# Optimization experiments

Measured on AMD Instinct MI355X. Metric: run time of the kernel, lower is better.

## Reference

```python
import jax, jax.numpy as jnp
import numpy as np

# ---- dims ----
B, NP_, NL = 32, 350, 30          # graphs, protein atoms, ligand atoms per graph
NG = NP_ + NL
N = B * NG                        # 12160 nodes
E = B * NP_ * NL                  # 336000 edges (dense bipartite per graph)
HID, HEADS, G = 128, 16, 20
DH = HID // HEADS
KV = 2 * HID + G                  # 276
R_MIN, R_MAX = 0.0, 10.0


def _mlp_params(key, din, dout, hid=HID):
    k1, k2 = jax.random.split(key)
    return (jax.random.normal(k1, (din, hid), jnp.float32) / np.sqrt(din),
            jnp.zeros((hid,), jnp.float32),
            jnp.ones((hid,), jnp.float32),
            jnp.zeros((hid,), jnp.float32),
            jax.random.normal(k2, (hid, dout), jnp.float32) / np.sqrt(hid),
            jnp.zeros((dout,), jnp.float32))


def setup_inputs() -> dict:
    key = jax.random.key(0)
    h = jax.random.normal(jax.random.fold_in(key, 0), (N, HID), jnp.float32)
    x = jax.random.normal(jax.random.fold_in(key, 1), (N, 3), jnp.float32) * 3.0
    # node layout per graph: NP_ protein atoms then NL ligand atoms
    mask_ligand = np.tile(np.concatenate([np.zeros(NP_, np.int64), np.ones(NL, np.int64)]), B)
    base = (np.arange(B) * NG)[:, None]
    prot = base + np.arange(NP_)[None, :]            # [B, NP_]
    lig = base + NP_ + np.arange(NL)[None, :]        # [B, NL]
    # torch: dst = repeat_interleave(protein, NL); src = ligand.repeat(NP_)
    dst = np.repeat(prot, NL, axis=1).reshape(-1)
    src = np.tile(lig, (1, NP_)).reshape(-1)
    inp = {"h": h, "x": x, "src": jnp.asarray(src), "dst": jnp.asarray(dst),
           "mask_ligand": jnp.asarray(mask_ligand)}
    dims = {"hk": (KV, HID), "hv": (KV, HID), "xv": (KV, HEADS), "hq": (HID, HID), "no": (2 * HID, HID)}
    for i, (nm, (di, do)) in enumerate(dims.items()):
        for s, arr in zip(("w1", "b1", "g", "be", "w2", "b2"), _mlp_params(jax.random.fold_in(key, 10 + i), di, do)):
            inp[f"{nm}_{s}"] = arr
    return inp


def _mlp(t, w1, b1, g, be, w2, b2):
    # Linear -> LayerNorm -> ReLU -> Linear
    y = t @ w1 + b1
    mu = y.mean(-1, keepdims=True)
    var = ((y - mu) ** 2).mean(-1, keepdims=True)
    y = jax.nn.relu((y - mu) * jax.lax.rsqrt(var + 1e-5) * g + be)
    return y @ w2 + b2


def _forward(h, x, src, dst, mask_ligand, ps):
    rel_x = x[src] - x[dst]                                   # [E,3]
    dist = jnp.linalg.norm(rel_x, axis=-1, keepdims=True)     # [E,1]
    offset = jnp.linspace(R_MIN, R_MAX, G)
    coeff = -0.5 / (offset[1] - offset[0]) ** 2
    r_feat = jnp.exp(coeff * (dist - offset) ** 2)            # [E,G]; outer_product(v) == v
    # inner layer unpacks (dst_i, src_i) = (src, dst): hi=h[src_i]=h[dst], hj=h[dst_i]=h[src]
    kv = jnp.concatenate([r_feat, h[dst], h[src]], -1)        # [E,KV]
    k = _mlp(kv, *ps["hk"]).reshape(-1, HEADS, DH)            # [E,H,dh]
    q = _mlp(h, *ps["hq"]).reshape(-1, HEADS, DH)             # [N,H,dh]
    logits = (q[src] * k).sum(-1) / np.sqrt(DH)               # [E,H]
    # scatter_softmax over dst_i = src groups (ligand nodes)
    smax = jax.ops.segment_max(logits, src, num_segments=N)
    ex = jnp.exp(logits - smax[src])
    alpha = ex / jax.ops.segment_sum(ex, src, num_segments=N)[src]   # [E,H]
    v = _mlp(kv, *ps["hv"]).reshape(-1, HEADS, DH)            # [E,H,dh]
    xv = _mlp(kv, *ps["xv"])                                  # [E,H]
    m = alpha[:, :, None] * v                                 # [E,H,dh]
    mx = (alpha * xv)[:, :, None] * rel_x[:, None, :]         # [E,H,3]
    out = jax.ops.segment_sum(m, src, num_segments=N).reshape(N, HID)
    out_x = jax.ops.segment_sum(mx, src, num_segments=N)      # [N,H,3]
    # out_fc: h_in[mask_ligand] with int64 mask gathers rows 0/1 (faithful to source)
    out = _mlp(jnp.concatenate([out, h[mask_ligand]], -1), *ps["no"])
    h_out = out + h
    x_out = x + out_x.mean(1)
    return h_out, x_out


def reference(h, x, src, dst, mask_ligand,
              hk_w1, hk_b1, hk_g, hk_be, hk_w2, hk_b2,
              hv_w1, hv_b1, hv_g, hv_be, hv_w2, hv_b2,
              xv_w1, xv_b1, xv_g, xv_be, xv_w2, xv_b2,
              hq_w1, hq_b1, hq_g, hq_be, hq_w2, hq_b2,
              no_w1, no_b1, no_g, no_be, no_w2, no_b2):
    ps = {"hk": (hk_w1, hk_b1, hk_g, hk_be, hk_w2, hk_b2),
          "hv": (hv_w1, hv_b1, hv_g, hv_be, hv_w2, hv_b2),
          "xv": (xv_w1, xv_b1, xv_g, xv_be, xv_w2, xv_b2),
          "hq": (hq_w1, hq_b1, hq_g, hq_be, hq_w2, hq_b2),
          "no": (no_w1, no_b1, no_g, no_be, no_w2, no_b2)}
    return _forward(h, x, src, dst, mask_ligand, ps)
```

## Files before the change

kernel.cpp:

```cpp
#include <hip/hip_runtime.h>
#include <math.h>

namespace {
constexpr int kB = 32;
constexpr int kNP = 350;
constexpr int kNL = 30;
constexpr int kNG = 380;
constexpr int kN = kB * kNG;
constexpr int kG = 20;
constexpr int kNPROT = kB * kNP;
constexpr int kNLIG = kB * kNL;
constexpr int TP = 32;
}

__global__ __launch_bounds__(256) void pre_kernel(
    const float* __restrict__ h,
    const float* __restrict__ wk1, const float* __restrict__ bk1,
    const float* __restrict__ wv1, const float* __restrict__ bv1,
    const float* __restrict__ wx1, const float* __restrict__ bx1,
    float* __restrict__ outKd, float* __restrict__ outVd, float* __restrict__ outXd,
    float* __restrict__ outKs, float* __restrict__ outVs, float* __restrict__ outXs) {
  const int m = blockIdx.y;
  const float* w1 = (m == 0) ? wk1 : (m == 1) ? wv1 : wx1;
  const float* b1 = (m == 0) ? bk1 : (m == 1) ? bv1 : bx1;
  const bool isProt = (blockIdx.x < 175);
  const int rbase = isProt ? blockIdx.x * 64 : (blockIdx.x - 175) * 64;
  float* outArr = isProt ? ((m == 0) ? outKd : (m == 1) ? outVd : outXd)
                         : ((m == 0) ? outKs : (m == 1) ? outVs : outXs);
  const float* wb = w1 + (isProt ? 20 * 128 : 148 * 128);

  __shared__ float sh[64 * 132];
  const int t = threadIdx.x;
#pragma unroll
  for (int j = 0; j < 8; ++j) {
    int flat = t + j * 256;
    int row = flat >> 5;
    int col = (flat & 31) * 4;
    int r = rbase + row;
    int node;
    if (isProt) node = (r / kNP) * kNG + (r % kNP);
    else        node = (r / kNL) * kNG + kNP + (r % kNL);
    *(float4*)&sh[row * 132 + col] = *(const float4*)(h + (size_t)node * 128 + col);
  }
  __syncthreads();

  const int dcol = (t & 31) * 4;
  const int rrow = (t >> 5) * 8;
  float4 acc[8];
#pragma unroll
  for (int i = 0; i < 8; ++i) acc[i] = make_float4(0.f, 0.f, 0.f, 0.f);

  for (int k = 0; k < 128; k += 4) {
    float4 a4[8];
#pragma unroll
    for (int i = 0; i < 8; ++i) a4[i] = *(float4*)&sh[(rrow + i) * 132 + k];
#pragma unroll
    for (int kk = 0; kk < 4; ++kk) {
      float4 w4 = *(const float4*)(wb + (size_t)(k + kk) * 128 + dcol);
#pragma unroll
      for (int i = 0; i < 8; ++i) {
        float a = (kk == 0) ? a4[i].x : (kk == 1) ? a4[i].y : (kk == 2) ? a4[i].z : a4[i].w;
        acc[i].x += a * w4.x; acc[i].y += a * w4.y;
        acc[i].z += a * w4.z; acc[i].w += a * w4.w;
      }
    }
  }
  float4 bias = make_float4(0.f, 0.f, 0.f, 0.f);
  if (!isProt) bias = *(const float4*)(b1 + dcol);
#pragma unroll
  for (int i = 0; i < 8; ++i) {
    float4 o = acc[i];
    o.x += bias.x; o.y += bias.y; o.z += bias.z; o.w += bias.w;
    *(float4*)(outArr + (size_t)(rbase + rrow + i) * 128 + dcol) = o;
  }
}

__global__ __launch_bounds__(128) void cvec_kernel(
    const float* __restrict__ h,
    const float* __restrict__ no_w1, const float* __restrict__ no_b1,
    const float* __restrict__ no_g, const float* __restrict__ no_be,
    const float* __restrict__ no_w2, const float* __restrict__ no_b2,
    float* __restrict__ cvec) {
  __shared__ float sy[128];
  __shared__ float sa[128];
  __shared__ float red[2];
  const int d = threadIdx.x;
  float y = no_b1[d];
  for (int i = 0; i < 128; ++i) y += h[i] * no_w1[(size_t)(128 + i) * 128 + d];
  sy[d] = y;
  __syncthreads();
  if (d == 0) {
    float s = 0.f, ss = 0.f;
    for (int i = 0; i < 128; ++i) { s += sy[i]; ss += sy[i] * sy[i]; }
    float mu = s / 128.f;
    red[0] = mu;
    red[1] = rsqrtf(ss / 128.f - mu * mu + 1e-5f);
  }
  __syncthreads();
  float a = (y - red[0]) * red[1] * no_g[d] + no_be[d];
  sa[d] = fmaxf(a, 0.f);
  __syncthreads();
  float o = no_b2[d];
  for (int i = 0; i < 128; ++i) o += sa[i] * no_w2[(size_t)i * 128 + d];
  cvec[d] = o;
}

__global__ __launch_bounds__(256) void prot_kernel(
    const float* __restrict__ h, const float* __restrict__ x,
    const float* __restrict__ cvec, float* __restrict__ hout, float* __restrict__ xout) {
  int idx = blockIdx.x * 256 + threadIdx.x;
  if (idx < kNPROT * 32) {
    int r = idx >> 5, c4 = (idx & 31) * 4;
    int node = (r / kNP) * kNG + (r % kNP);
    float4 hv = *(const float4*)(h + (size_t)node * 128 + c4);
    float4 cv = *(const float4*)(cvec + c4);
    *(float4*)(hout + (size_t)node * 128 + c4) =
        make_float4(hv.x + cv.x, hv.y + cv.y, hv.z + cv.z, hv.w + cv.w);
  }
  if (idx < kNPROT * 3) {
    int r = idx / 3, c = idx % 3;
    int node = (r / kNP) * kNG + (r % kNP);
    xout[(size_t)node * 3 + c] = x[(size_t)node * 3 + c];
  }
}

__global__ __launch_bounds__(256, 2) void edge_kernel(
    const float* __restrict__ h, const float* __restrict__ x,
    const float* __restrict__ preKd, const float* __restrict__ preVd, const float* __restrict__ preXd,
    const float* __restrict__ preKs, const float* __restrict__ preVs, const float* __restrict__ preXs,
    const float* __restrict__ hk_w1, const float* __restrict__ hk_g, const float* __restrict__ hk_be,
    const float* __restrict__ hk_w2, const float* __restrict__ hk_b2,
    const float* __restrict__ hv_w1, const float* __restrict__ hv_g, const float* __restrict__ hv_be,
    const float* __restrict__ hv_w2, const float* __restrict__ hv_b2,
    const float* __restrict__ xv_w1, const float* __restrict__ xv_g, const float* __restrict__ xv_be,
    const float* __restrict__ xv_w2, const float* __restrict__ xv_b2,
    const float* __restrict__ hq_w1, const float* __restrict__ hq_b1, const float* __restrict__ hq_g,
    const float* __restrict__ hq_be, const float* __restrict__ hq_w2, const float* __restrict__ hq_b2,
    const float* __restrict__ no_w1, const float* __restrict__ no_b1, const float* __restrict__ no_g,
    const float* __restrict__ no_be, const float* __restrict__ no_w2, const float* __restrict__ no_b2,
    float* __restrict__ hout, float* __restrict__ xout) {

  __shared__ float smem[16180];
  float* const s_pres  = smem;
  float* const s_qb    = smem + 384;
  float* const s_qw    = smem + 400;
  float* const s_logit = smem + 2512;
  float* const s_a     = smem + 8112;
  float* const s_rfu   = smem + 12336;
  float* const s_q     = s_rfu;
  float* const s_outv  = s_rfu + 128;
  float* const s_outx  = s_rfu + 256;
  float* const s_mx    = s_rfu + 320;
  float* const s_sum   = s_rfu + 336;
  float* const s_rx    = smem + 12976;
  float* const s_w1r   = smem + 13104;
  float* const s_wx    = smem + 15664;
  float* const s_tmp   = s_wx;
  float* const s_red   = smem + 16176;

  const int wg = blockIdx.x;
  const int g = wg / kNL, l = wg % kNL;
  const int lignode = g * kNG + kNP + l;
  const int ligidx = g * kNL + l;
  const int t = threadIdx.x;
  const int lane = t & 63;
  const int wv = t >> 6;
  const int myd4 = (t & 31) * 4;
  const int myp = t >> 5;

  for (int i = t; i < 640; i += 256)
    *(float4*)&s_w1r[i * 4] = *(const float4*)(hk_w1 + i * 4);
  if (t < 32) *(float4*)&s_tmp[t * 4] = *(const float4*)(h + (size_t)lignode * 128 + t * 4);
  if (t >= 64 && t < 160) {
    int i = t - 64, m = i >> 5, c4 = (i & 31) * 4;
    const float* src = (m == 0) ? preKs : (m == 1) ? preVs : preXs;
    *(float4*)&s_pres[m * 128 + c4] = *(const float4*)(src + (size_t)ligidx * 128 + c4);
  }
  __syncthreads();

  float yq = 0.f;
  if (t < 128) {
    yq = hq_b1[t];
    for (int k = 0; k < 128; ++k) yq += s_tmp[k] * hq_w1[(size_t)k * 128 + t];
    s_a[t] = yq;
  }
  __syncthreads();
  if (t < 64) {
    float v0 = s_a[t], v1 = s_a[t + 64];
    float s = v0 + v1, ss = v0 * v0 + v1 * v1;
#pragma unroll
    for (int off = 32; off; off >>= 1) { s += __shfl_xor(s, off); ss += __shfl_xor(ss, off); }
    if (t == 0) {
      float mu = s / 128.f;
      s_red[0] = mu;
      s_red[1] = rsqrtf(ss / 128.f - mu * mu + 1e-5f);
    }
  }
  __syncthreads();
  if (t < 128) {
    float a = (yq - s_red[0]) * s_red[1] * hq_g[t] + hq_be[t];
    s_tmp[t] = fmaxf(a, 0.f);
  }
  __syncthreads();
  if (t < 128) {
    float qv = hq_b2[t];
    for (int d = 0; d < 128; ++d) qv += s_tmp[d] * hq_w2[(size_t)d * 128 + t];
    s_q[t] = qv;
  }
  __syncthreads();

  constexpr float kInvSqrtDH = 0.35355339059327379f;
#pragma unroll
  for (int i = 0; i < 8; ++i) {
    int idx = t + i * 256;
    int hh = idx >> 7, d = idx & 127;
    float4 wa = *(const float4*)(hk_w2 + (size_t)d * 128 + hh * 8);
    float4 wb = *(const float4*)(hk_w2 + (size_t)d * 128 + hh * 8 + 4);
    float v = wa.x * s_q[hh * 8 + 0] + wa.y * s_q[hh * 8 + 1] + wa.z * s_q[hh * 8 + 2] +
              wa.w * s_q[hh * 8 + 3] + wb.x * s_q[hh * 8 + 4] + wb.y * s_q[hh * 8 + 5] +
              wb.z * s_q[hh * 8 + 6] + wb.w * s_q[hh * 8 + 7];
    s_qw[hh * 132 + d] = v * kInvSqrtDH;
  }
  if (t < 16) {
    float v = 0.f;
#pragma unroll
    for (int j = 0; j < 8; ++j) v += hk_b2[t * 8 + j] * s_q[t * 8 + j];
    s_qb[t] = v * kInvSqrtDH;
  }
  const float lx0 = x[(size_t)lignode * 3 + 0];
  const float lx1 = x[(size_t)lignode * 3 + 1];
  const float lx2 = x[(size_t)lignode * 3 + 2];
  __syncthreads();

  constexpr float kStep = 10.f / 19.f;
  constexpr float kCoeff = -0.5f / (kStep * kStep);

  for (int tile = 0; tile < 11; ++tile) {
    const int p0 = tile * TP;
    const int np = (350 - p0) < TP ? (350 - p0) : TP;
    if (t < np) {
      int p = p0 + t;
      const float* xp = x + (size_t)(g * kNG + p) * 3;
      float r0 = lx0 - xp[0], r1 = lx1 - xp[1], r2 = lx2 - xp[2];
      float dist = sqrtf(r0 * r0 + r1 * r1 + r2 * r2);
#pragma unroll
      for (int gg = 0; gg < kG; ++gg) {
        float dd = dist - gg * kStep;
        s_rfu[t * 20 + gg] = __expf(kCoeff * dd * dd);
      }
    }
    __syncthreads();
    for (int i = myp; i < np; i += 8) {
      const float* prow = preKd + (size_t)(g * kNP + p0 + i) * 128;
      float4 yv = *(float4*)&s_pres[0 * 128 + myd4];
      float4 pr = *(const float4*)(prow + myd4);
      yv.x += pr.x; yv.y += pr.y; yv.z += pr.z; yv.w += pr.w;
#pragma unroll
      for (int gg = 0; gg < kG; ++gg) {
        float r = s_rfu[i * 20 + gg];
        float4 w4 = *(float4*)&s_w1r[gg * 128 + myd4];
        yv.x += r * w4.x; yv.y += r * w4.y; yv.z += r * w4.z; yv.w += r * w4.w;
      }
      *(float4*)&s_a[i * 132 + myd4] = yv;
    }
    __syncthreads();
    for (int rr = wv; rr < np; rr += 4) {
      float v0 = s_a[rr * 132 + lane], v1 = s_a[rr * 132 + lane + 64];
      float s = v0 + v1, ss = v0 * v0 + v1 * v1;
#pragma unroll
      for (int off = 32; off; off >>= 1) { s += __shfl_xor(s, off); ss += __shfl_xor(ss, off); }
      float mu = s * (1.f / 128.f);
      float rs = rsqrtf(ss * (1.f / 128.f) - mu * mu + 1e-5f);
      s_a[rr * 132 + lane] = fmaxf((v0 - mu) * rs * hk_g[lane] + hk_be[lane], 0.f);
      s_a[rr * 132 + lane + 64] =
          fmaxf((v1 - mu) * rs * hk_g[lane + 64] + hk_be[lane + 64], 0.f);
    }
    __syncthreads();
    for (int o = t; o < np * 16; o += 256) {
      int p = o >> 4, hh = o & 15;
      float acc = 0.f;
#pragma unroll
      for (int d = 0; d < 128; d += 4) {
        float4 a4 = *(float4*)&s_a[p * 132 + d];
        float4 w4 = *(float4*)&s_qw[hh * 132 + d];
        acc += a4.x * w4.x + a4.y * w4.y + a4.z * w4.z + a4.w * w4.w;
      }
      s_logit[(p0 + p) * 16 + hh] = acc + s_qb[hh];
    }
    __syncthreads();
  }

  {
    int hh = t & 15, ck = t >> 4;
    float mx = -1e30f;
    for (int p = ck; p < 350; p += 16) mx = fmaxf(mx, s_logit[p * 16 + hh]);
    s_tmp[t] = mx;
  }
  __syncthreads();
  if (t < 16) {
    float mx = s_tmp[t];
    for (int c = 1; c < 16; ++c) mx = fmaxf(mx, s_tmp[c * 16 + t]);
    s_mx[t] = mx;
  }
  __syncthreads();
  {
    int hh = t & 15, ck = t >> 4;
    float mx = s_mx[hh], sm = 0.f;
    for (int p = ck; p < 350; p += 16) sm += __expf(s_logit[p * 16 + hh] - mx);
    s_tmp[t] = sm;
  }
  __syncthreads();
  if (t < 16) {
    float sm = 0.f;
    for (int c = 0; c < 16; ++c) sm += s_tmp[c * 16 + t];
    s_sum[t] = 1.f / sm;
  }
  __syncthreads();
  for (int o = t; o < 350 * 16; o += 256) {
    int hh = o & 15;
    s_logit[o] = __expf(s_logit[o] - s_mx[hh]) * s_sum[hh];
  }
  __syncthreads();
  for (int i = t; i < 640; i += 256)
    *(float4*)&s_w1r[i * 4] = *(const float4*)(hv_w1 + i * 4);
  for (int o = t; o < 2048; o += 256) {
    int hh = o >> 7, d = o & 127;
    s_qw[hh * 132 + d] = xv_w2[(size_t)d * 16 + hh];
  }
  __syncthreads();

  float acc_v[8];
#pragma unroll
  for (int i = 0; i < 8; ++i) acc_v[i] = 0.f;
  const int dd = t & 127;
  const int hb8 = (t >> 7) * 8;

  for (int tile = 0; tile < 11; ++tile) {
    const int p0 = tile * TP;
    const int np = (350 - p0) < TP ? (350 - p0) : TP;
    if (t < np) {
      int p = p0 + t;
      const float* xp = x + (size_t)(g * kNG + p) * 3;
      float r0 = lx0 - xp[0], r1 = lx1 - xp[1], r2 = lx2 - xp[2];
      float dist = sqrtf(r0 * r0 + r1 * r1 + r2 * r2);
#pragma unroll
      for (int gg = 0; gg < kG; ++gg) {
        float dd2 = dist - gg * kStep;
        s_rfu[t * 20 + gg] = __expf(kCoeff * dd2 * dd2);
      }
    }
    __syncthreads();
    for (int i = myp; i < np; i += 8) {
      const float* prow = preVd + (size_t)(g * kNP + p0 + i) * 128;
      float4 yv = *(float4*)&s_pres[1 * 128 + myd4];
      float4 pr = *(const float4*)(prow + myd4);
      yv.x += pr.x; yv.y += pr.y; yv.z += pr.z; yv.w += pr.w;
#pragma unroll
      for (int gg = 0; gg < kG; ++gg) {
        float r = s_rfu[i * 20 + gg];
        float4 w4 = *(float4*)&s_w1r[gg * 128 + myd4];
        yv.x += r * w4.x; yv.y += r * w4.y; yv.z += r * w4.z; yv.w += r * w4.w;
      }
      *(float4*)&s_a[i * 132 + myd4] = yv;
    }
    __syncthreads();
    for (int rr = wv; rr < np; rr += 4) {
      float v0 = s_a[rr * 132 + lane], v1 = s_a[rr * 132 + lane + 64];
      float s = v0 + v1, ss = v0 * v0 + v1 * v1;
#pragma unroll
      for (int off = 32; off; off >>= 1) { s += __shfl_xor(s, off); ss += __shfl_xor(ss, off); }
      float mu = s * (1.f / 128.f);
      float rs = rsqrtf(ss * (1.f / 128.f) - mu * mu + 1e-5f);
      s_a[rr * 132 + lane] = fmaxf((v0 - mu) * rs * hv_g[lane] + hv_be[lane], 0.f);
      s_a[rr * 132 + lane + 64] =
          fmaxf((v1 - mu) * rs * hv_g[lane + 64] + hv_be[lane + 64], 0.f);
    }
    __syncthreads();
    for (int p = 0; p < np; ++p) {
      float av = s_a[p * 132 + dd];
      const float* al = &s_logit[(p0 + p) * 16 + hb8];
#pragma unroll
      for (int i = 0; i < 8; ++i) acc_v[i] += al[i] * av;
    }
    __syncthreads();
  }

  for (int i = t; i < 640; i += 256)
    *(float4*)&s_w1r[i * 4] = *(const float4*)(xv_w1 + i * 4);
  __syncthreads();

  float accx = 0.f;
  for (int tile = 0; tile < 11; ++tile) {
    const int p0 = tile * TP;
    const int np = (350 - p0) < TP ? (350 - p0) : TP;
    if (t < np) {
      int p = p0 + t;
      const float* xp = x + (size_t)(g * kNG + p) * 3;
      float r0 = lx0 - xp[0], r1 = lx1 - xp[1], r2 = lx2 - xp[2];
      float dist = sqrtf(r0 * r0 + r1 * r1 + r2 * r2);
      s_rx[t * 4 + 0] = r0; s_rx[t * 4 + 1] = r1; s_rx[t * 4 + 2] = r2;
#pragma unroll
      for (int gg = 0; gg < kG; ++gg) {
        float dd2 = dist - gg * kStep;
        s_rfu[t * 20 + gg] = __expf(kCoeff * dd2 * dd2);
      }
    }
    __syncthreads();
    for (int i = myp; i < np; i += 8) {
      const float* prow = preXd + (size_t)(g * kNP + p0 + i) * 128;
      float4 yv = *(float4*)&s_pres[2 * 128 + myd4];
      float4 pr = *(const float4*)(prow + myd4);
      yv.x += pr.x; yv.y += pr.y; yv.z += pr.z; yv.w += pr.w;
#pragma unroll
      for (int gg = 0; gg < kG; ++gg) {
        float r = s_rfu[i * 20 + gg];
        float4 w4 = *(float4*)&s_w1r[gg * 128 + myd4];
        yv.x += r * w4.x; yv.y += r * w4.y; yv.z += r * w4.z; yv.w += r * w4.w;
      }
      *(float4*)&s_a[i * 132 + myd4] = yv;
    }
    __syncthreads();
    for (int rr = wv; rr < np; rr += 4) {
      float v0 = s_a[rr * 132 + lane], v1 = s_a[rr * 132 + lane + 64];
      float s = v0 + v1, ss = v0 * v0 + v1 * v1;
#pragma unroll
      for (int off = 32; off; off >>= 1) { s += __shfl_xor(s, off); ss += __shfl_xor(ss, off); }
      float mu = s * (1.f / 128.f);
      float rs = rsqrtf(ss * (1.f / 128.f) - mu * mu + 1e-5f);
      s_a[rr * 132 + lane] = fmaxf((v0 - mu) * rs * xv_g[lane] + xv_be[lane], 0.f);
      s_a[rr * 132 + lane + 64] =
          fmaxf((v1 - mu) * rs * xv_g[lane + 64] + xv_be[lane + 64], 0.f);
    }
    __syncthreads();
    for (int o = t; o < np * 16; o += 256) {
      int p = o >> 4, hh = o & 15;
      float acc = xv_b2[hh];
#pragma unroll
      for (int d = 0; d < 128; d += 4) {
        float4 a4 = *(float4*)&s_a[p * 132 + d];
        float4 w4 = *(float4*)&s_qw[hh * 132 + d];
        acc += a4.x * w4.x + a4.y * w4.y + a4.z * w4.z + a4.w * w4.w;
      }
      s_wx[p * 16 + hh] = s_logit[(p0 + p) * 16 + hh] * acc;
    }
    __syncthreads();
    if (t < 48) {
      int hh = t / 3, c = t % 3;
      float sm = 0.f;
      for (int p = 0; p < np; ++p) sm += s_wx[p * 16 + hh] * s_rx[p * 4 + c];
      accx += sm;
    }
    __syncthreads();
  }

#pragma unroll
  for (int i = 0; i < 8; ++i) s_a[(hb8 + i) * 132 + dd] = acc_v[i];
  if (t < 48) s_outx[(t / 3) * 4 + (t % 3)] = accx;
  __syncthreads();

  if (t < 128) {
    float o = hv_b2[t];
    const int hh = t >> 3;
    for (int d = 0; d < 128; ++d) o += s_a[hh * 132 + d] * hv_w2[(size_t)d * 128 + t];
    s_outv[t] = o;
  }
  __syncthreads();
  if (t < 3) {
    float sm = 0.f;
#pragma unroll
    for (int hh = 0; hh < 16; ++hh) sm += s_outx[hh * 4 + t];
    xout[(size_t)lignode * 3 + t] = x[(size_t)lignode * 3 + t] + sm * (1.f / 16.f);
  }
  float yn = 0.f;
  if (t < 128) {
    yn = no_b1[t];
    for (int i = 0; i < 128; ++i) yn += s_outv[i] * no_w1[(size_t)i * 128 + t];
    const float* h1 = h + 128;
    for (int i = 0; i < 128; ++i) yn += h1[i] * no_w1[(size_t)(128 + i) * 128 + t];
    s_tmp[t] = yn;
  }
  __syncthreads();
  if (t < 64) {
    float v0 = s_tmp[t], v1 = s_tmp[t + 64];
    float s = v0 + v1, ss = v0 * v0 + v1 * v1;
#pragma unroll
    for (int off = 32; off; off >>= 1) { s += __shfl_xor(s, off); ss += __shfl_xor(ss, off); }
    if (t == 0) {
      float mu = s / 128.f;
      s_red[0] = mu;
      s_red[1] = rsqrtf(ss / 128.f - mu * mu + 1e-5f);
    }
  }
  __syncthreads();
  if (t < 128) {
    float a = (yn - s_red[0]) * s_red[1] * no_g[t] + no_be[t];
    s_outv[t] = fmaxf(a, 0.f);
  }
  __syncthreads();
  if (t < 128) {
    float o = no_b2[t];
    for (int d = 0; d < 128; ++d) o += s_outv[d] * no_w2[(size_t)d * 128 + t];
    hout[(size_t)lignode * 128 + t] = o + h[(size_t)lignode * 128 + t];
  }
}

extern "C" void kernel_launch(void* const* d_in, const int* in_sizes, int n_in,
                              void* d_out, int out_size, void* d_ws, size_t ws_size,
                              hipStream_t stream) {
  (void)in_sizes; (void)n_in; (void)out_size; (void)ws_size;
  const float* h = (const float*)d_in[0];
  const float* x = (const float*)d_in[1];
  const float* hk_w1 = (const float*)d_in[5];
  const float* hk_b1 = (const float*)d_in[6];
  const float* hk_g  = (const float*)d_in[7];
  const float* hk_be = (const float*)d_in[8];
  const float* hk_w2 = (const float*)d_in[9];
  const float* hk_b2 = (const float*)d_in[10];
  const float* hv_w1 = (const float*)d_in[11];
  const float* hv_b1 = (const float*)d_in[12];
  const float* hv_g  = (const float*)d_in[13];
  const float* hv_be = (const float*)d_in[14];
  const float* hv_w2 = (const float*)d_in[15];
  const float* hv_b2 = (const float*)d_in[16];
  const float* xv_w1 = (const float*)d_in[17];
  const float* xv_b1 = (const float*)d_in[18];
  const float* xv_g  = (const float*)d_in[19];
  const float* xv_be = (const float*)d_in[20];
  const float* xv_w2 = (const float*)d_in[21];
  const float* xv_b2 = (const float*)d_in[22];
  const float* hq_w1 = (const float*)d_in[23];
  const float* hq_b1 = (const float*)d_in[24];
  const float* hq_g  = (const float*)d_in[25];
  const float* hq_be = (const float*)d_in[26];
  const float* hq_w2 = (const float*)d_in[27];
  const float* hq_b2 = (const float*)d_in[28];
  const float* no_w1 = (const float*)d_in[29];
  const float* no_b1 = (const float*)d_in[30];
  const float* no_g  = (const float*)d_in[31];
  const float* no_be = (const float*)d_in[32];
  const float* no_w2 = (const float*)d_in[33];
  const float* no_b2 = (const float*)d_in[34];

  float* ws = (float*)d_ws;
  float* preKd = ws;
  float* preVd = preKd + (size_t)kNPROT * 128;
  float* preXd = preVd + (size_t)kNPROT * 128;
  float* preKs = preXd + (size_t)kNPROT * 128;
  float* preVs = preKs + (size_t)kNLIG * 128;
  float* preXs = preVs + (size_t)kNLIG * 128;
  float* cvec  = preXs + (size_t)kNLIG * 128;

  float* hout = (float*)d_out;
  float* xout = hout + (size_t)kN * 128;

  pre_kernel<<<dim3(190, 3), dim3(256), 0, stream>>>(
      h, hk_w1, hk_b1, hv_w1, hv_b1, xv_w1, xv_b1,
      preKd, preVd, preXd, preKs, preVs, preXs);
  cvec_kernel<<<dim3(1), dim3(128), 0, stream>>>(
      h, no_w1, no_b1, no_g, no_be, no_w2, no_b2, cvec);
  edge_kernel<<<dim3(960), dim3(256), 0, stream>>>(
      h, x, preKd, preVd, preXd, preKs, preVs, preXs,
      hk_w1, hk_g, hk_be, hk_w2, hk_b2,
      hv_w1, hv_g, hv_be, hv_w2, hv_b2,
      xv_w1, xv_g, xv_be, xv_w2, xv_b2,
      hq_w1, hq_b1, hq_g, hq_be, hq_w2, hq_b2,
      no_w1, no_b1, no_g, no_be, no_w2, no_b2,
      hout, xout);
  prot_kernel<<<dim3(1400), dim3(256), 0, stream>>>(h, x, cvec, hout, xout);
}
```

Baseline: 768.9 us.

## Fuse LayerNorm into edge MLP pass, keep weights in registers, cut barriers

The three per-edge MLP loops now keep the 20x4 radial-weight slice in registers instead of shared memory. LayerNorm and ReLU are fused into the first-layer accumulation through 32-lane shuffle reductions, which removes a separate normalisation pass and its barrier. Distances are computed once per block, and the RBF features for the next tile are computed in the same phase as the current logit pass. The x-update reduction uses warp shuffles rather than a serial 48-thread loop. Shared memory shrinks and the launch bound rises to 3 blocks per CU, which increases register pressure and the risk of spills.

```diff
diff --git a/kernel.cpp b/kernel.cpp
--- a/kernel.cpp
+++ b/kernel.cpp
@@ -11,6 +11,7 @@
 constexpr int kNPROT = kB * kNP;
 constexpr int kNLIG = kB * kNL;
 constexpr int TP = 32;
+constexpr int NT = 11;
 }
 
 __global__ __launch_bounds__(256) void pre_kernel(
@@ -124,7 +125,7 @@
   }
 }
 
-__global__ __launch_bounds__(256, 2) void edge_kernel(
+__global__ __launch_bounds__(256, 3) void edge_kernel(
     const float* __restrict__ h, const float* __restrict__ x,
     const float* __restrict__ preKd, const float* __restrict__ preVd, const float* __restrict__ preXd,
     const float* __restrict__ preKs, const float* __restrict__ preVs, const float* __restrict__ preXs,
@@ -140,41 +141,41 @@
     const float* __restrict__ no_be, const float* __restrict__ no_w2, const float* __restrict__ no_b2,
     float* __restrict__ hout, float* __restrict__ xout) {
 
-  __shared__ float smem[16180];
-  float* const s_pres  = smem;
-  float* const s_qb    = smem + 384;
-  float* const s_qw    = smem + 400;
-  float* const s_logit = smem + 2512;
-  float* const s_a     = smem + 8112;
-  float* const s_rfu   = smem + 12336;
+  __shared__ float smem[13236];
+  float* const s_qw    = smem;
+  float* const s_logit = smem + 2112;
+  float* const s_a     = smem + 7712;
+  float* const s_rfu   = smem + 11936;
   float* const s_q     = s_rfu;
   float* const s_outv  = s_rfu + 128;
   float* const s_outx  = s_rfu + 256;
-  float* const s_mx    = s_rfu + 320;
-  float* const s_sum   = s_rfu + 336;
-  float* const s_rx    = smem + 12976;
-  float* const s_w1r   = smem + 13104;
-  float* const s_wx    = smem + 15664;
-  float* const s_tmp   = s_wx;
-  float* const s_red   = smem + 16176;
+  float* const s_dist  = smem + 12576;
+  float* const s_tmp   = smem + 12928;
+  float* const s_qb    = smem + 13184;
+  float* const s_mx    = smem + 13200;
+  float* const s_sum   = smem + 13216;
+  float* const s_red   = smem + 13232;
 
   const int wg = blockIdx.x;
   const int g = wg / kNL, l = wg % kNL;
   const int lignode = g * kNG + kNP + l;
   const int ligidx = g * kNL + l;
   const int t = threadIdx.x;
-  const int lane = t & 63;
-  const int wv = t >> 6;
-  const int myd4 = (t & 31) * 4;
+  const int c4 = (t & 31) * 4;
   const int myp = t >> 5;
 
-  for (int i = t; i < 640; i += 256)
-    *(float4*)&s_w1r[i * 4] = *(const float4*)(hk_w1 + i * 4);
+  constexpr float kStep = 10.f / 19.f;
+  constexpr float kCoeff = -0.5f / (kStep * kStep);
+
+  const float lx0 = x[(size_t)lignode * 3 + 0];
+  const float lx1 = x[(size_t)lignode * 3 + 1];
+  const float lx2 = x[(size_t)lignode * 3 + 2];
+
   if (t < 32) *(float4*)&s_tmp[t * 4] = *(const float4*)(h + (size_t)lignode * 128 + t * 4);
-  if (t >= 64 && t < 160) {
-    int i = t - 64, m = i >> 5, c4 = (i & 31) * 4;
-    const float* src = (m == 0) ? preKs : (m == 1) ? preVs : preXs;
-    *(float4*)&s_pres[m * 128 + c4] = *(const float4*)(src + (size_t)ligidx * 128 + c4);
+  for (int p = t; p < kNP; p += 256) {
+    const float* xp = x + (size_t)(g * kNG + p) * 3;
+    float r0 = lx0 - xp[0], r1 = lx1 - xp[1], r2 = lx2 - xp[2];
+    s_dist[p] = sqrtf(r0 * r0 + r1 * r1 + r2 * r2);
   }
   __syncthreads();
 
@@ -227,67 +228,85 @@
     for (int j = 0; j < 8; ++j) v += hk_b2[t * 8 + j] * s_q[t * 8 + j];
     s_qb[t] = v * kInvSqrtDH;
   }
-  const float lx0 = x[(size_t)lignode * 3 + 0];
-  const float lx1 = x[(size_t)lignode * 3 + 1];
-  const float lx2 = x[(size_t)lignode * 3 + 2];
-  __syncthreads();
-
-  constexpr float kStep = 10.f / 19.f;
-  constexpr float kCoeff = -0.5f / (kStep * kStep);
-
-  for (int tile = 0; tile < 11; ++tile) {
-    const int p0 = tile * TP;
-    const int np = (350 - p0) < TP ? (350 - p0) : TP;
-    if (t < np) {
-      int p = p0 + t;
-      const float* xp = x + (size_t)(g * kNG + p) * 3;
-      float r0 = lx0 - xp[0], r1 = lx1 - xp[1], r2 = lx2 - xp[2];
-      float dist = sqrtf(r0 * r0 + r1 * r1 + r2 * r2);
-#pragma unroll
-      for (int gg = 0; gg < kG; ++gg) {
-        float dd = dist - gg * kStep;
-        s_rfu[t * 20 + gg] = __expf(kCoeff * dd * dd);
-      }
+  for (int o = t; o < TP * 20; o += 256) {
+    int p = o / 20;
+    float dd = s_dist[p] - (o - p * 20) * kStep;
+    s_rfu[o] = __expf(kCoeff * dd * dd);
+  }
+  __syncthreads();
+
+  {
+    float4 w1r[20];
+#pragma unroll
+    for (int gg = 0; gg < 20; ++gg) w1r[gg] = *(const float4*)(hk_w1 + gg * 128 + c4);
+    const float4 g4 = *(const float4*)(hk_g + c4);
+    const float4 be4 = *(const float4*)(hk_be + c4);
+    const float4 pres4 = *(const float4*)(preKs + (size_t)ligidx * 128 + c4);
+
+    for (int tile = 0; tile < NT; ++tile) {
+      const int p0 = tile * TP;
+      const int np = (350 - p0) < TP ? (350 - p0) : TP;
+      float4 pr[4];
+#pragma unroll
+      for (int r = 0; r < 4; ++r) {
+        int i = myp + r * 8;
+        if (i < np) pr[r] = *(const float4*)(preKd + (size_t)(g * kNP + p0 + i) * 128 + c4);
+      }
+#pragma unroll
+      for (int r = 0; r < 4; ++r) {
+        int i = myp + r * 8;
+        if (i < np) {
+          float4 yv;
+          yv.x = pres4.x + pr[r].x; yv.y = pres4.y + pr[r].y;
+          yv.z = pres4.z + pr[r].z; yv.w = pres4.w + pr[r].w;
+#pragma unroll
+          for (int gg = 0; gg < 20; ++gg) {
+            float rf = s_rfu[i * 20 + gg];
+            yv.x += rf * w1r[gg].x; yv.y += rf * w1r[gg].y;
+            yv.z += rf * w1r[gg].z; yv.w += rf * w1r[gg].w;
+          }
+          float s = yv.x + yv.y + yv.z + yv.w;
+          float ss = yv.x * yv.x + yv.y * yv.y + yv.z * yv.z + yv.w * yv.w;
+#pragma unroll
+          for (int m = 16; m; m >>= 1) { s += __shfl_xor(s, m); ss += __shfl_xor(ss, m); }
+          float mu = s * (1.f / 128.f);
+          float rs = rsqrtf(ss * (1.f / 128.f) - mu * mu + 1e-5f);
+          float4 a;
+          a.x = fmaxf((yv.x - mu) * rs * g4.x + be4.x, 0.f);
+          a.y = fmaxf((yv.y - mu) * rs * g4.y + be4.y, 0.f);
+          a.z = fmaxf((yv.z - mu) * rs * g4.z + be4.z, 0.f);
+          a.w = fmaxf((yv.w - mu) * rs * g4.w + be4.w, 0.f);
+          *(float4*)&s_a[i * 132 + c4] = a;
+        }
+      }
+      __syncthreads();
+      {
+        const int p = t & 31;
+        const int h0 = (t >> 5) * 2, h1 = h0 + 1;
+        float f0 = 0.f, f1 = 0.f;
+#pragma unroll
+        for (int d = 0; d < 128; d += 4) {
+          float4 a4 = *(float4*)&s_a[p * 132 + d];
+          float4 q0 = *(float4*)&s_qw[h0 * 132 + d];
+          float4 q1 = *(float4*)&s_qw[h1 * 132 + d];
+          f0 += a4.x * q0.x + a4.y * q0.y + a4.z * q0.z + a4.w * q0.w;
+          f1 += a4.x * q1.x + a4.y * q1.y + a4.z * q1.z + a4.w * q1.w;
+        }
+        if (p < np) {
+          s_logit[(p0 + p) * 16 + h0] = f0 + s_qb[h0];
+          s_logit[(p0 + p) * 16 + h1] = f1 + s_qb[h1];
+        }
+        const int nxt = (tile + 1 == NT) ? 0 : tile + 1;
+        const int q0p = nxt * TP;
+        const int nq = (350 - q0p) < TP ? (350 - q0p) : TP;
+        for (int o = t; o < nq * 20; o += 256) {
+          int pp = o / 20;
+          float dd = s_dist[q0p + pp] - (o - pp * 20) * kStep;
+          s_rfu[o] = __expf(kCoeff * dd * dd);
+        }
+      }
+      __syncthreads();
     }
-    __syncthreads();
-    for (int i = myp; i < np; i += 8) {
-      const float* prow = preKd + (size_t)(g * kNP + p0 + i) * 128;
-      float4 yv = *(float4*)&s_pres[0 * 128 + myd4];
-      float4 pr = *(const float4*)(prow + myd4);
-      yv.x += pr.x; yv.y += pr.y; yv.z += pr.z; yv.w += pr.w;
-#pragma unroll
-      for (int gg = 0; gg < kG; ++gg) {
-        float r = s_rfu[i * 20 + gg];
-        float4 w4 = *(float4*)&s_w1r[gg * 128 + myd4];
-        yv.x += r * w4.x; yv.y += r * w4.y; yv.z += r * w4.z; yv.w += r * w4.w;
-      }
-      *(float4*)&s_a[i * 132 + myd4] = yv;
-    }
-    __syncthreads();
-    for (int rr = wv; rr < np; rr += 4) {
-      float v0 = s_a[rr * 132 + lane], v1 = s_a[rr * 132 + lane + 64];
-      float s = v0 + v1, ss = v0 * v0 + v1 * v1;
-#pragma unroll
-      for (int off = 32; off; off >>= 1) { s += __shfl_xor(s, off); ss += __shfl_xor(ss, off); }
-      float mu = s * (1.f / 128.f);
-      float rs = rsqrtf(ss * (1.f / 128.f) - mu * mu + 1e-5f);
-      s_a[rr * 132 + lane] = fmaxf((v0 - mu) * rs * hk_g[lane] + hk_be[lane], 0.f);
-      s_a[rr * 132 + lane + 64] =
-          fmaxf((v1 - mu) * rs * hk_g[lane + 64] + hk_be[lane + 64], 0.f);
-    }
-    __syncthreads();
-    for (int o = t; o < np * 16; o += 256) {
-      int p = o >> 4, hh = o & 15;
-      float acc = 0.f;
-#pragma unroll
-      for (int d = 0; d < 128; d += 4) {
-        float4 a4 = *(float4*)&s_a[p * 132 + d];
-        float4 w4 = *(float4*)&s_qw[hh * 132 + d];
-        acc += a4.x * w4.x + a4.y * w4.y + a4.z * w4.z + a4.w * w4.w;
-      }
-      s_logit[(p0 + p) * 16 + hh] = acc + s_qb[hh];
-    }
-    __syncthreads();
   }
 
   {
@@ -320,142 +339,188 @@
     int hh = o & 15;
     s_logit[o] = __expf(s_logit[o] - s_mx[hh]) * s_sum[hh];
   }
-  __syncthreads();
-  for (int i = t; i < 640; i += 256)
-    *(float4*)&s_w1r[i * 4] = *(const float4*)(hv_w1 + i * 4);
   for (int o = t; o < 2048; o += 256) {
     int hh = o >> 7, d = o & 127;
     s_qw[hh * 132 + d] = xv_w2[(size_t)d * 16 + hh];
   }
-  __syncthreads();
-
-  float acc_v[8];
-#pragma unroll
-  for (int i = 0; i < 8; ++i) acc_v[i] = 0.f;
-  const int dd = t & 127;
+  if (t < 16) s_qb[t] = xv_b2[t];
+  __syncthreads();
+
+  float accv[8];
+#pragma unroll
+  for (int i = 0; i < 8; ++i) accv[i] = 0.f;
+  const int dd_ = t & 127;
   const int hb8 = (t >> 7) * 8;
-
-  for (int tile = 0; tile < 11; ++tile) {
-    const int p0 = tile * TP;
-    const int np = (350 - p0) < TP ? (350 - p0) : TP;
-    if (t < np) {
-      int p = p0 + t;
-      const float* xp = x + (size_t)(g * kNG + p) * 3;
-      float r0 = lx0 - xp[0], r1 = lx1 - xp[1], r2 = lx2 - xp[2];
-      float dist = sqrtf(r0 * r0 + r1 * r1 + r2 * r2);
-#pragma unroll
-      for (int gg = 0; gg < kG; ++gg) {
-        float dd2 = dist - gg * kStep;
-        s_rfu[t * 20 + gg] = __expf(kCoeff * dd2 * dd2);
-      }
+  {
+    float4 w1r[20];
+#pragma unroll
+    for (int gg = 0; gg < 20; ++gg) w1r[gg] = *(const float4*)(hv_w1 + gg * 128 + c4);
+    const float4 g4 = *(const float4*)(hv_g + c4);
+    const float4 be4 = *(const float4*)(hv_be + c4);
+    const float4 pres4 = *(const float4*)(preVs + (size_t)ligidx * 128 + c4);
+
+    for (int tile = 0; tile < NT; ++tile) {
+      const int p0 = tile * TP;
+      const int np = (350 - p0) < TP ? (350 - p0) : TP;
+      float4 pr[4];
+#pragma unroll
+      for (int r = 0; r < 4; ++r) {
+        int i = myp + r * 8;
+        if (i < np) pr[r] = *(const float4*)(preVd + (size_t)(g * kNP + p0 + i) * 128 + c4);
+      }
+#pragma unroll
+      for (int r = 0; r < 4; ++r) {
+        int i = myp + r * 8;
+        if (i < np) {
+          float4 yv;
+          yv.x = pres4.x + pr[r].x; yv.y = pres4.y + pr[r].y;
+          yv.z = pres4.z + pr[r].z; yv.w = pres4.w + pr[r].w;
+#pragma unroll
+          for (int gg = 0; gg < 20; ++gg) {
+            float rf = s_rfu[i * 20 + gg];
+            yv.x += rf * w1r[gg].x; yv.y += rf * w1r[gg].y;
+            yv.z += rf * w1r[gg].z; yv.w += rf * w1r[gg].w;
+          }
+          float s = yv.x + yv.y + yv.z + yv.w;
+          float ss = yv.x * yv.x + yv.y * yv.y + yv.z * yv.z + yv.w * yv.w;
+#pragma unroll
+          for (int m = 16; m; m >>= 1) { s += __shfl_xor(s, m); ss += __shfl_xor(ss, m); }
+          float mu = s * (1.f / 128.f);
+          float rs = rsqrtf(ss * (1.f / 128.f) - mu * mu + 1e-5f);
+          float4 a;
+          a.x = fmaxf((yv.x - mu) * rs * g4.x + be4.x, 0.f);
+          a.y = fmaxf((yv.y - mu) * rs * g4.y + be4.y, 0.f);
+          a.z = fmaxf((yv.z - mu) * rs * g4.z + be4.z, 0.f);
+          a.w = fmaxf((yv.w - mu) * rs * g4.w + be4.w, 0.f);
+          *(float4*)&s_a[i * 132 + c4] = a;
+        }
+      }
+      __syncthreads();
+      for (int p = 0; p < np; ++p) {
+        float av = s_a[p * 132 + dd_];
+        float4 alA = *(float4*)&s_logit[(p0 + p) * 16 + hb8];
+        float4 alB = *(float4*)&s_logit[(p0 + p) * 16 + hb8 + 4];
+        accv[0] += alA.x * av; accv[1] += alA.y * av;
+        accv[2] += alA.z * av; accv[3] += alA.w * av;
+        accv[4] += alB.x * av; accv[5] += alB.y * av;
+        accv[6] += alB.z * av; accv[7] += alB.w * av;
+      }
+      {
+        const int nxt = (tile + 1 == NT) ? 0 : tile + 1;
+        const int q0p = nxt * TP;
+        const int nq = (350 - q0p) < TP ? (350 - q0p) : TP;
+        for (int o = t; o < nq * 20; o += 256) {
+          int pp = o / 20;
+          float dd2 = s_dist[q0p + pp] - (o - pp * 20) * kStep;
+          s_rfu[o] = __expf(kCoeff * dd2 * dd2);
+        }
+      }
+      __syncthreads();
     }
-    __syncthreads();
-    for (int i = myp; i < np; i += 8) {
-      const float* prow = preVd + (size_t)(g * kNP + p0 + i) * 128;
-      float4 yv = *(float4*)&s_pres[1 * 128 + myd4];
-      float4 pr = *(const float4*)(prow + myd4);
-      yv.x += pr.x; yv.y += pr.y; yv.z += pr.z; yv.w += pr.w;
-#pragma unroll
-      for (int gg = 0; gg < kG; ++gg) {
-        float r = s_rfu[i * 20 + gg];
-        float4 w4 = *(float4*)&s_w1r[gg * 128 + myd4];
-        yv.x += r * w4.x; yv.y += r * w4.y; yv.z += r * w4.z; yv.w += r * w4.w;
-      }
-      *(float4*)&s_a[i * 132 + myd4] = yv;
+  }
+
+  float ax[6];
+#pragma unroll
+  for (int i = 0; i < 6; ++i) ax[i] = 0.f;
+  {
+    float4 w1r[20];
+#pragma unroll
+    for (int gg = 0; gg < 20; ++gg) w1r[gg] = *(const float4*)(xv_w1 + gg * 128 + c4);
+    const float4 g4 = *(const float4*)(xv_g + c4);
+    const float4 be4 = *(const float4*)(xv_be + c4);
+    const float4 pres4 = *(const float4*)(preXs + (size_t)ligidx * 128 + c4);
+    const int p_ = t & 31;
+    const int h0 = (t >> 5) * 2, h1 = h0 + 1;
+
+    for (int tile = 0; tile < NT; ++tile) {
+      const int p0 = tile * TP;
+      const int np = (350 - p0) < TP ? (350 - p0) : TP;
+      float4 pr[4];
+#pragma unroll
+      for (int r = 0; r < 4; ++r) {
+        int i = myp + r * 8;
+        if (i < np) pr[r] = *(const float4*)(preXd + (size_t)(g * kNP + p0 + i) * 128 + c4);
+      }
+#pragma unroll
+      for (int r = 0; r < 4; ++r) {
+        int i = myp + r * 8;
+        if (i < np) {
+          float4 yv;
+          yv.x = pres4.x + pr[r].x; yv.y = pres4.y + pr[r].y;
+          yv.z = pres4.z + pr[r].z; yv.w = pres4.w + pr[r].w;
+#pragma unroll
+          for (int gg = 0; gg < 20; ++gg) {
+            float rf = s_rfu[i * 20 + gg];
+            yv.x += rf * w1r[gg].x; yv.y += rf * w1r[gg].y;
+            yv.z += rf * w1r[gg].z; yv.w += rf * w1r[gg].w;
+          }
+          float s = yv.x + yv.y + yv.z + yv.w;
+          float ss = yv.x * yv.x + yv.y * yv.y + yv.z * yv.z + yv.w * yv.w;
+#pragma unroll
+          for (int m = 16; m; m >>= 1) { s += __shfl_xor(s, m); ss += __shfl_xor(ss, m); }
+          float mu = s * (1.f / 128.f);
+          float rs = rsqrtf(ss * (1.f / 128.f) - mu * mu + 1e-5f);
+          float4 a;
+          a.x = fmaxf((yv.x - mu) * rs * g4.x + be4.x, 0.f);
+          a.y = fmaxf((yv.y - mu) * rs * g4.y + be4.y, 0.f);
+          a.z = fmaxf((yv.z - mu) * rs * g4.z + be4.z, 0.f);
+          a.w = fmaxf((yv.w - mu) * rs * g4.w + be4.w, 0.f);
+          *(float4*)&s_a[i * 132 + c4] = a;
+        }
+      }
+      __syncthreads();
+      {
+        float f0 = 0.f, f1 = 0.f;
+#pragma unroll
+        for (int d = 0; d < 128; d += 4) {
+          float4 a4 = *(float4*)&s_a[p_ * 132 + d];
+          float4 q0 = *(float4*)&s_qw[h0 * 132 + d];
+          float4 q1 = *(float4*)&s_qw[h1 * 132 + d];
+          f0 += a4.x * q0.x + a4.y * q0.y + a4.z * q0.z + a4.w * q0.w;
+          f1 += a4.x * q1.x + a4.y * q1.y + a4.z * q1.z + a4.w * q1.w;
+        }
+        float w0 = 0.f, w1 = 0.f, r0 = 0.f, r1 = 0.f, r2 = 0.f;
+        if (p_ < np) {
+          int pg = p0 + p_;
+          w0 = s_logit[pg * 16 + h0] * (f0 + s_qb[h0]);
+          w1 = s_logit[pg * 16 + h1] * (f1 + s_qb[h1]);
+          const float* xp = x + (size_t)(g * kNG + pg) * 3;
+          r0 = lx0 - xp[0]; r1 = lx1 - xp[1]; r2 = lx2 - xp[2];
+        }
+        float p00 = w0 * r0, p01 = w0 * r1, p02 = w0 * r2;
+        float p10 = w1 * r0, p11 = w1 * r1, p12 = w1 * r2;
+#pragma unroll
+        for (int m = 16; m; m >>= 1) {
+          p00 += __shfl_xor(p00, m); p01 += __shfl_xor(p01, m); p02 += __shfl_xor(p02, m);
+          p10 += __shfl_xor(p10, m); p11 += __shfl_xor(p11, m); p12 += __shfl_xor(p12, m);
+        }
+        ax[0] += p00; ax[1] += p01; ax[2] += p02;
+        ax[3] += p10; ax[4] += p11; ax[5] += p12;
+      }
+      {
+        const int nxt = (tile + 1 == NT) ? 0 : tile + 1;
+        const int q0p = nxt * TP;
+        const int nq = (350 - q0p) < TP ? (350 - q0p) : TP;
+        for (int o = t; o < nq * 20; o += 256) {
+          int pp = o / 20;
+          float dd2 = s_dist[q0p + pp] - (o - pp * 20) * kStep;
+          s_rfu[o] = __expf(kCoeff * dd2 * dd2);
+        }
+      }
+      __syncthreads();
     }
-    __syncthreads();
-    for (int rr = wv; rr < np; rr += 4) {
-      float v0 = s_a[rr * 132 + lane], v1 = s_a[rr * 132 + lane + 64];
-      float s = v0 + v1, ss = v0 * v0 + v1 * v1;
-#pragma unroll
-      for (int off = 32; off; off >>= 1) { s += __shfl_xor(s, off); ss += __shfl_xor(ss, off); }
-      float mu = s * (1.f / 128.f);
-      float rs = rsqrtf(ss * (1.f / 128.f) - mu * mu + 1e-5f);
-      s_a[rr * 132 + lane] = fmaxf((v0 - mu) * rs * hv_g[lane] + hv_be[lane], 0.f);
-      s_a[rr * 132 + lane + 64] =
-          fmaxf((v1 - mu) * rs * hv_g[lane + 64] + hv_be[lane + 64], 0.f);
+  }
+
+#pragma unroll
+  for (int i = 0; i < 8; ++i) s_a[(hb8 + i) * 132 + dd_] = accv[i];
+  {
+    const int h0 = (t >> 5) * 2;
+    if ((t & 31) == 0) {
+      s_outx[h0 * 4 + 0] = ax[0]; s_outx[h0 * 4 + 1] = ax[1]; s_outx[h0 * 4 + 2] = ax[2];
+      s_outx[(h0 + 1) * 4 + 0] = ax[3]; s_outx[(h0 + 1) * 4 + 1] = ax[4];
+      s_outx[(h0 + 1) * 4 + 2] = ax[5];
     }
-    __syncthreads();
-    for (int p = 0; p < np; ++p) {
-      float av = s_a[p * 132 + dd];
-      const float* al = &s_logit[(p0 + p) * 16 + hb8];
-#pragma unroll
-      for (int i = 0; i < 8; ++i) acc_v[i] += al[i] * av;
-    }
-    __syncthreads();
-  }
-
-  for (int i = t; i < 640; i += 256)
-    *(float4*)&s_w1r[i * 4] = *(const float4*)(xv_w1 + i * 4);
-  __syncthreads();
-
-  float accx = 0.f;
-  for (int tile = 0; tile < 11; ++tile) {
-    const int p0 = tile * TP;
-    const int np = (350 - p0) < TP ? (350 - p0) : TP;
-    if (t < np) {
-      int p = p0 + t;
-      const float* xp = x + (size_t)(g * kNG + p) * 3;
-      float r0 = lx0 - xp[0], r1 = lx1 - xp[1], r2 = lx2 - xp[2];
-      float dist = sqrtf(r0 * r0 + r1 * r1 + r2 * r2);
-      s_rx[t * 4 + 0] = r0; s_rx[t * 4 + 1] = r1; s_rx[t * 4 + 2] = r2;
-#pragma unroll
-      for (int gg = 0; gg < kG; ++gg) {
-        float dd2 = dist - gg * kStep;
-        s_rfu[t * 20 + gg] = __expf(kCoeff * dd2 * dd2);
-      }
-    }
-    __syncthreads();
-    for (int i = myp; i < np; i += 8) {
-      const float* prow = preXd + (size_t)(g * kNP + p0 + i) * 128;
-      float4 yv = *(float4*)&s_pres[2 * 128 + myd4];
-      float4 pr = *(const float4*)(prow + myd4);
-      yv.x += pr.x; yv.y += pr.y; yv.z += pr.z; yv.w += pr.w;
-#pragma unroll
-      for (int gg = 0; gg < kG; ++gg) {
-        float r = s_rfu[i * 20 + gg];
-        float4 w4 = *(float4*)&s_w1r[gg * 128 + myd4];
-        yv.x += r * w4.x; yv.y += r * w4.y; yv.z += r * w4.z; yv.w += r * w4.w;
-      }
-      *(float4*)&s_a[i * 132 + myd4] = yv;
-    }
-    __syncthreads();
-    for (int rr = wv; rr < np; rr += 4) {
-      float v0 = s_a[rr * 132 + lane], v1 = s_a[rr * 132 + lane + 64];
-      float s = v0 + v1, ss = v0 * v0 + v1 * v1;
-#pragma unroll
-      for (int off = 32; off; off >>= 1) { s += __shfl_xor(s, off); ss += __shfl_xor(ss, off); }
-      float mu = s * (1.f / 128.f);
-      float rs = rsqrtf(ss * (1.f / 128.f) - mu * mu + 1e-5f);
-      s_a[rr * 132 + lane] = fmaxf((v0 - mu) * rs * xv_g[lane] + xv_be[lane], 0.f);
-      s_a[rr * 132 + lane + 64] =
-          fmaxf((v1 - mu) * rs * xv_g[lane + 64] + xv_be[lane + 64], 0.f);
-    }
-    __syncthreads();
-    for (int o = t; o < np * 16; o += 256) {
-      int p = o >> 4, hh = o & 15;
-      float acc = xv_b2[hh];
-#pragma unroll
-      for (int d = 0; d < 128; d += 4) {
-        float4 a4 = *(float4*)&s_a[p * 132 + d];
-        float4 w4 = *(float4*)&s_qw[hh * 132 + d];
-        acc += a4.x * w4.x + a4.y * w4.y + a4.z * w4.z + a4.w * w4.w;
-      }
-      s_wx[p * 16 + hh] = s_logit[(p0 + p) * 16 + hh] * acc;
-    }
-    __syncthreads();
-    if (t < 48) {
-      int hh = t / 3, c = t % 3;
-      float sm = 0.f;
-      for (int p = 0; p < np; ++p) sm += s_wx[p * 16 + hh] * s_rx[p * 4 + c];
-      accx += sm;
-    }
-    __syncthreads();
-  }
-
-#pragma unroll
-  for (int i = 0; i < 8; ++i) s_a[(hb8 + i) * 132 + dd] = acc_v[i];
-  if (t < 48) s_outx[(t / 3) * 4 + (t % 3)] = accx;
+  }
   __syncthreads();
 
   if (t < 128) {
@@ -464,13 +529,14 @@
     for (int d = 0; d < 128; ++d) o += s_a[hh * 132 + d] * hv_w2[(size_t)d * 128 + t];
     s_outv[t] = o;
   }
-  __syncthreads();
-  if (t < 3) {
+  if (t >= 128 && t < 131) {
+    int c = t - 128;
     float sm = 0.f;
 #pragma unroll
-    for (int hh = 0; hh < 16; ++hh) sm += s_outx[hh * 4 + t];
-    xout[(size_t)lignode * 3 + t] = x[(size_t)lignode * 3 + t] + sm * (1.f / 16.f);
-  }
+    for (int hh = 0; hh < 16; ++hh) sm += s_outx[hh * 4 + c];
+    xout[(size_t)lignode * 3 + c] = x[(size_t)lignode * 3 + c] + sm * (1.f / 16.f);
+  }
+  __syncthreads();
   float yn = 0.f;
   if (t < 128) {
     yn = no_b1[t];
```

New measurement: 1.043 ms. +35.7%, slower.
